# Optimization experiments

Hardware: AMD Instinct MI355X
Metric: run time of the kernel (lower is better)

## Reference

```python
import jax, jax.numpy as jnp
import numpy as np

N_NODES = 50000
N_EDGES = 800000
IN_CH, HIDDEN, OUT_CH = 64, 16, 8


def setup_inputs() -> dict:
    key = jax.random.key(0)
    ks = jax.random.split(key, 8)
    x = jax.random.normal(ks[0], (N_NODES, IN_CH), dtype=jnp.float32)
    edge_index = jax.random.randint(ks[1], (2, N_EDGES), 0, N_NODES, dtype=jnp.int64)
    # SAGEConv params: lin_l (neighbor aggregate, has bias), lin_r (root, no bias)
    s1 = 1.0 / np.sqrt(IN_CH)
    s2 = 1.0 / np.sqrt(HIDDEN)
    W1l = jax.random.uniform(ks[2], (HIDDEN, IN_CH), jnp.float32, -s1, s1)
    W1r = jax.random.uniform(ks[3], (HIDDEN, IN_CH), jnp.float32, -s1, s1)
    b1 = jax.random.uniform(ks[4], (HIDDEN,), jnp.float32, -s1, s1)
    W2l = jax.random.uniform(ks[5], (OUT_CH, HIDDEN), jnp.float32, -s2, s2)
    W2r = jax.random.uniform(ks[6], (OUT_CH, HIDDEN), jnp.float32, -s2, s2)
    b2 = jax.random.uniform(ks[7], (OUT_CH,), jnp.float32, -s2, s2)
    return {"x": x, "W1l": W1l, "W1r": W1r, "b1": b1,
            "W2l": W2l, "W2r": W2r, "b2": b2, "edge_index": edge_index}


def _sage_conv(x, src, dst, Wl, Wr, b, n_nodes):
    # mean-aggregate neighbor features: gather from src, scatter-mean to dst
    msg_sum = jax.ops.segment_sum(x[src], dst, num_segments=n_nodes)  # [N, d]
    deg = jax.ops.segment_sum(jnp.ones((src.shape[0], 1), x.dtype), dst,
                              num_segments=n_nodes)                    # [N, 1]
    aggr = msg_sum / jnp.maximum(deg, 1.0)
    # out = lin_l(aggr) + lin_r(x); bias lives in lin_l
    return aggr @ Wl.T + x @ Wr.T + b


def reference(x, W1l, W1r, b1, W2l, W2r, b2, edge_index):
    src, dst = edge_index[0], edge_index[1]
    n = x.shape[0]
    h = jax.nn.relu(_sage_conv(x, src, dst, W1l, W1r, b1, n))
    # F.dropout(p=0.1, training=self.training): identity in eval mode
    return _sage_conv(h, src, dst, W2l, W2r, b2, n)
```

## Files before the change

kernel.cpp:

```cpp
#include <hip/hip_runtime.h>

#define IN_CH 64
#define HID   16
#define OUTC  8
#define BINSHIFT 6
#define BINCAP  (1 << BINSHIFT)
#define CHUNK   2048

typedef _Float16 half2_t __attribute__((ext_vector_type(2)));
typedef _Float16 half8_t __attribute__((ext_vector_type(8)));


__global__ __launch_bounds__(256) void build_xform(
    const float* __restrict__ x,
    const int*   __restrict__ esrc,
    const int*   __restrict__ edst,
    const float* __restrict__ W1l,
    const float* __restrict__ W1r,
    const float* __restrict__ b1,
    int* __restrict__ cur,
    unsigned short* __restrict__ adj,
    _Float16* __restrict__ y1h,
    float* __restrict__ r1,
    int n_nodes, int n_edges, int nb_scatter)
{
    __shared__ __align__(16) float sWl[HID * 68];
    __shared__ __align__(16) float sWr[HID * 68];
    __shared__ __align__(16) float sx[16 * 68];
    __shared__ float sb1[HID];

    int b   = blockIdx.x;
    int tid = threadIdx.x;

    if (b < nb_scatter) {
        int slice = b & 7;
        int chunk = b >> 3;
        int lo = (int)(((long long)slice       * n_nodes) >> 3);
        int hi = (int)(((long long)(slice + 1) * n_nodes) >> 3);
        int base = chunk * CHUNK;
#pragma unroll
        for (int j = 0; j < CHUNK / 256; ++j) {
            int e = base + j * 256 + tid;
            if (e < n_edges) {
                int d = edst[e];
                if (d >= lo && d < hi) {
                    int pos = atomicAdd(&cur[d], 1);
                    if (pos < BINCAP)
                        adj[((size_t)d << BINSHIFT) + pos] =
                            (unsigned short)esrc[e];
                }
            }
        }
        return;
    }

    for (int i = tid; i < HID * IN_CH; i += 256) {
        int c = i >> 6, k = i & 63;
        sWl[c * 68 + k] = W1l[i];
        sWr[c * 68 + k] = W1r[i];
    }
    if (tid < HID) sb1[tid] = b1[tid];

    int nl   = tid >> 4;
    int c    = tid & 15;
    int node = (b - nb_scatter) * 16 + nl;

    if (node < n_nodes)
        *(float4*)&sx[nl * 68 + c * 4] =
            *(const float4*)&x[(size_t)node * IN_CH + c * 4];
    __syncthreads();
    if (node >= n_nodes) return;

    float accL = 0.f, accR = 0.f;
#pragma unroll
    for (int k4 = 0; k4 < 16; ++k4) {
        float4 xv = *(const float4*)&sx [nl * 68 + k4 * 4];
        float4 wl = *(const float4*)&sWl[c  * 68 + k4 * 4];
        float4 wr = *(const float4*)&sWr[c  * 68 + k4 * 4];
        accL = fmaf(xv.x, wl.x, accL); accL = fmaf(xv.y, wl.y, accL);
        accL = fmaf(xv.z, wl.z, accL); accL = fmaf(xv.w, wl.w, accL);
        accR = fmaf(xv.x, wr.x, accR); accR = fmaf(xv.y, wr.y, accR);
        accR = fmaf(xv.z, wr.z, accR); accR = fmaf(xv.w, wr.w, accR);
    }
    y1h[(size_t)node * HID + c] = (_Float16)accL;
    r1 [(size_t)node * HID + c] = accR + sb1[c];
}

#define ACC8(v)                                                          \
    do {                                                                 \
        half2_t p01 = {(v).s0, (v).s1}, p23 = {(v).s2, (v).s3};          \
        half2_t p45 = {(v).s4, (v).s5}, p67 = {(v).s6, (v).s7};          \
        s0 = __builtin_amdgcn_fdot2(p01, k10, s0, false);                \
        s1 = __builtin_amdgcn_fdot2(p01, k01, s1, false);                \
        s2 = __builtin_amdgcn_fdot2(p23, k10, s2, false);                \
        s3 = __builtin_amdgcn_fdot2(p23, k01, s3, false);                \
        s4 = __builtin_amdgcn_fdot2(p45, k10, s4, false);                \
        s5 = __builtin_amdgcn_fdot2(p45, k01, s5, false);                \
        s6 = __builtin_amdgcn_fdot2(p67, k10, s6, false);                \
        s7 = __builtin_amdgcn_fdot2(p67, k01, s7, false);                \
    } while (0)

__global__ __launch_bounds__(256) void fused_gather(
    const float* __restrict__ r1,
    const _Float16* __restrict__ y1h,
    const int*   __restrict__ cur,
    const unsigned short* __restrict__ adj,
    const float* __restrict__ W2l, const float* __restrict__ W2r,
    const float* __restrict__ b2,
    _Float16* __restrict__ y2h, float* __restrict__ r2out,
    int n_nodes)
{
    __shared__ float sW2l[HID * OUTC];
    __shared__ float sW2r[HID * OUTC];
    __shared__ float sb2[OUTC];
    __shared__ float sh[32 * 17];

    int tid = threadIdx.x;
    for (int i = tid; i < HID * OUTC; i += 256) {
        int o = i >> 4, k = i & 15;
        sW2l[k * OUTC + o] = W2l[i];
        sW2r[k * OUTC + o] = W2r[i];
    }
    if (tid < OUTC) sb2[tid] = b2[tid];

    int nl   = tid >> 3;
    int t    = tid & 7;
    int h    = t >> 2;
    int ep   = t & 3;
    int node = blockIdx.x * 32 + nl;
    bool real = node < n_nodes;

    const half2_t k10 = {(_Float16)1.f, (_Float16)0.f};
    const half2_t k01 = {(_Float16)0.f, (_Float16)1.f};

    if (real) {
        int deg = cur[node];
        if (deg > BINCAP) deg = BINCAP;
        int iters = deg >> 2;
        float s0 = 0.f, s1 = 0.f, s2 = 0.f, s3 = 0.f;
        float s4 = 0.f, s5 = 0.f, s6 = 0.f, s7 = 0.f;
        const _Float16* yq = y1h + h * 8;
        const unsigned short* row = adj + ((size_t)node << BINSHIFT);
        const ushort4* ap = (const ushort4*)row;
        for (int it = ep; it < iters; it += 4) {
            ushort4 s = ap[it];
            half8_t v0 = *(const half8_t*)(yq + (size_t)s.x * HID);
            half8_t v1 = *(const half8_t*)(yq + (size_t)s.y * HID);
            half8_t v2 = *(const half8_t*)(yq + (size_t)s.z * HID);
            half8_t v3 = *(const half8_t*)(yq + (size_t)s.w * HID);
            ACC8(v0); ACC8(v1); ACC8(v2); ACC8(v3);
        }
        for (int g = (iters << 2) + ep; g < deg; g += 4) {
            half8_t v = *(const half8_t*)(yq + (size_t)row[g] * HID);
            ACC8(v);
        }
        s0 += __shfl_xor(s0, 1); s0 += __shfl_xor(s0, 2);
        s1 += __shfl_xor(s1, 1); s1 += __shfl_xor(s1, 2);
        s2 += __shfl_xor(s2, 1); s2 += __shfl_xor(s2, 2);
        s3 += __shfl_xor(s3, 1); s3 += __shfl_xor(s3, 2);
        s4 += __shfl_xor(s4, 1); s4 += __shfl_xor(s4, 2);
        s5 += __shfl_xor(s5, 1); s5 += __shfl_xor(s5, 2);
        s6 += __shfl_xor(s6, 1); s6 += __shfl_xor(s6, 2);
        s7 += __shfl_xor(s7, 1); s7 += __shfl_xor(s7, 2);

        if (ep == 0) {
            float inv = 1.0f / fmaxf((float)deg, 1.0f);
            const float* rr = &r1[(size_t)node * HID + h * 8];
            float4 ra = *(const float4*)(rr);
            float4 rb = *(const float4*)(rr + 4);
            float* shp = &sh[nl * 17 + h * 8];
            shp[0] = fmaxf(fmaf(s0, inv, ra.x), 0.f);
            shp[1] = fmaxf(fmaf(s1, inv, ra.y), 0.f);
            shp[2] = fmaxf(fmaf(s2, inv, ra.z), 0.f);
            shp[3] = fmaxf(fmaf(s3, inv, ra.w), 0.f);
            shp[4] = fmaxf(fmaf(s4, inv, rb.x), 0.f);
            shp[5] = fmaxf(fmaf(s5, inv, rb.y), 0.f);
            shp[6] = fmaxf(fmaf(s6, inv, rb.z), 0.f);
            shp[7] = fmaxf(fmaf(s7, inv, rb.w), 0.f);
        }
    }
    __syncthreads();
    if (!real) return;

    const float* hrow = &sh[nl * 17];
    float al = 0.f, ar = sb2[t];
#pragma unroll
    for (int k = 0; k < HID; ++k) {
        float hv = hrow[k];
        al = fmaf(hv, sW2l[k * OUTC + t], al);
        ar = fmaf(hv, sW2r[k * OUTC + t], ar);
    }
    y2h[(size_t)node * OUTC + t] = (_Float16)al;
    r2out[(size_t)node * OUTC + t] = ar;
}

__global__ __launch_bounds__(256) void gather_out(
    const _Float16* __restrict__ y2h,
    const int*   __restrict__ cur,
    const unsigned short* __restrict__ adj,
    float* __restrict__ out,
    int n_nodes)
{
    int tid  = threadIdx.x;
    int node = blockIdx.x * 64 + (tid >> 2);
    if (node >= n_nodes) return;
    int ep = tid & 3;

    int deg = cur[node];
    if (deg > BINCAP) deg = BINCAP;
    int iters = deg >> 2;
    const unsigned short* row = adj + ((size_t)node << BINSHIFT);
    const ushort4* ap = (const ushort4*)row;

    const half2_t k10 = {(_Float16)1.f, (_Float16)0.f};
    const half2_t k01 = {(_Float16)0.f, (_Float16)1.f};

    float s0 = 0.f, s1 = 0.f, s2 = 0.f, s3 = 0.f;
    float s4 = 0.f, s5 = 0.f, s6 = 0.f, s7 = 0.f;
    for (int it = ep; it < iters; it += 4) {
        ushort4 s = ap[it];
        half8_t v0 = *(const half8_t*)(y2h + (size_t)s.x * OUTC);
        half8_t v1 = *(const half8_t*)(y2h + (size_t)s.y * OUTC);
        half8_t v2 = *(const half8_t*)(y2h + (size_t)s.z * OUTC);
        half8_t v3 = *(const half8_t*)(y2h + (size_t)s.w * OUTC);
        ACC8(v0); ACC8(v1); ACC8(v2); ACC8(v3);
    }
    for (int g = (iters << 2) + ep; g < deg; g += 4) {
        half8_t v = *(const half8_t*)(y2h + (size_t)row[g] * OUTC);
        ACC8(v);
    }
    s0 += __shfl_xor(s0, 1); s0 += __shfl_xor(s0, 2);
    s1 += __shfl_xor(s1, 1); s1 += __shfl_xor(s1, 2);
    s2 += __shfl_xor(s2, 1); s2 += __shfl_xor(s2, 2);
    s3 += __shfl_xor(s3, 1); s3 += __shfl_xor(s3, 2);
    s4 += __shfl_xor(s4, 1); s4 += __shfl_xor(s4, 2);
    s5 += __shfl_xor(s5, 1); s5 += __shfl_xor(s5, 2);
    s6 += __shfl_xor(s6, 1); s6 += __shfl_xor(s6, 2);
    s7 += __shfl_xor(s7, 1); s7 += __shfl_xor(s7, 2);
    if (ep != 0) return;

    float inv = 1.0f / fmaxf((float)deg, 1.0f);
    float* op = out + (size_t)node * OUTC;
    float4 c0 = *(float4*)op;
    float4 c1 = *(float4*)(op + 4);
    c0.x = fmaf(s0, inv, c0.x); c0.y = fmaf(s1, inv, c0.y);
    c0.z = fmaf(s2, inv, c0.z); c0.w = fmaf(s3, inv, c0.w);
    c1.x = fmaf(s4, inv, c1.x); c1.y = fmaf(s5, inv, c1.y);
    c1.z = fmaf(s6, inv, c1.z); c1.w = fmaf(s7, inv, c1.w);
    *(float4*)op = c0;
    *(float4*)(op + 4) = c1;
}

extern "C" void kernel_launch(void* const* d_in, const int* in_sizes, int n_in,
                              void* d_out, int out_size, void* d_ws, size_t ws_size,
                              hipStream_t stream)
{
    const float* x   = (const float*)d_in[0];
    const float* W1l = (const float*)d_in[1];
    const float* W1r = (const float*)d_in[2];
    const float* b1  = (const float*)d_in[3];
    const float* W2l = (const float*)d_in[4];
    const float* W2r = (const float*)d_in[5];
    const float* b2  = (const float*)d_in[6];
    const int*   ei  = (const int*)d_in[7];

    int n_nodes = in_sizes[0] / IN_CH;
    int n_edges = in_sizes[7] / 2;
    const int* esrc = ei;
    const int* edst = ei + n_edges;

    float* out = (float*)d_out;

    char* wsb = (char*)d_ws;
    _Float16* y1h = (_Float16*)wsb;
    _Float16* y2h = y1h + (size_t)n_nodes * HID;
    float* r1 = (float*)(y2h + (size_t)n_nodes * OUTC);
    int* cur  = (int*)(r1 + (size_t)n_nodes * HID);
    unsigned short* adj = (unsigned short*)(cur + n_nodes);

    dim3 blk(256);
    int n_chunks   = (n_edges + CHUNK - 1) / CHUNK;
    int nb_scatter = n_chunks * 8;
    int nb_node    = (n_nodes + 15) / 16;

    hipMemsetAsync(cur, 0, (size_t)n_nodes * sizeof(int), stream);

    build_xform<<<dim3(nb_scatter + nb_node), blk, 0, stream>>>(
        x, esrc, edst, W1l, W1r, b1, cur, adj, y1h, r1,
        n_nodes, n_edges, nb_scatter);

    fused_gather<<<dim3((n_nodes + 31) / 32), blk, 0, stream>>>(
        r1, y1h, cur, adj, W2l, W2r, b2, y2h, out, n_nodes);

    gather_out<<<dim3((n_nodes + 63) / 64), blk, 0, stream>>>(
        y2h, cur, adj, out, n_nodes);
}
```

Before: 132.2 us.

## Replace per-node global atomics with two-pass slice partitioning for adjacency build

Edge scatter becomes a two-level counting sort. Partition blocks first histogram destinations into 256-node slices in shared memory, then reserve space with one global atomic per slice and write packed (src, local dst) words into per-slice buffers. A new bin_build kernel then builds each slice's fixed-capacity adjacency bins in LDS and writes them out with coalesced stores. This removes the repeated 8x read of the edge list and the per-edge global atomics on cur, at the cost of an extra kernel launch and an intermediate buffer. It also relies on gcnt having exactly 256 entries, one per slice (ns=196 here), and on slices not overflowing BCAP.

```diff
diff --git a/kernel.cpp b/kernel.cpp
--- a/kernel.cpp
+++ b/kernel.cpp
@@ -5,7 +5,11 @@
 #define OUTC  8
 #define BINSHIFT 6
 #define BINCAP  (1 << BINSHIFT)
-#define CHUNK   2048
+
+#define CHUNK_A     4096
+#define SLICE_SHIFT 8
+#define SLICE_NODES 256
+#define BCAP        6144
 
 typedef _Float16 half2_t __attribute__((ext_vector_type(2)));
 typedef _Float16 half8_t __attribute__((ext_vector_type(8)));
@@ -18,37 +22,48 @@
     const float* __restrict__ W1l,
     const float* __restrict__ W1r,
     const float* __restrict__ b1,
-    int* __restrict__ cur,
-    unsigned short* __restrict__ adj,
+    int* __restrict__ gcnt,
+    unsigned int* __restrict__ gbuf,
     _Float16* __restrict__ y1h,
     float* __restrict__ r1,
-    int n_nodes, int n_edges, int nb_scatter)
+    int n_nodes, int n_edges, int nb_part)
 {
     __shared__ __align__(16) float sWl[HID * 68];
     __shared__ __align__(16) float sWr[HID * 68];
     __shared__ __align__(16) float sx[16 * 68];
     __shared__ float sb1[HID];
+    __shared__ int shist[SLICE_NODES];
+    __shared__ int scurs[SLICE_NODES];
 
     int b   = blockIdx.x;
     int tid = threadIdx.x;
 
-    if (b < nb_scatter) {
-        int slice = b & 7;
-        int chunk = b >> 3;
-        int lo = (int)(((long long)slice       * n_nodes) >> 3);
-        int hi = (int)(((long long)(slice + 1) * n_nodes) >> 3);
-        int base = chunk * CHUNK;
+    if (b < nb_part) {
+        int base = b * CHUNK_A;
+        shist[tid] = 0;
+        __syncthreads();
 #pragma unroll
-        for (int j = 0; j < CHUNK / 256; ++j) {
+        for (int j = 0; j < CHUNK_A / 256; ++j) {
+            int e = base + j * 256 + tid;
+            if (e < n_edges)
+                atomicAdd(&shist[edst[e] >> SLICE_SHIFT], 1);
+        }
+        __syncthreads();
+        int h = shist[tid];
+        if (h) scurs[tid] = atomicAdd(&gcnt[tid], h);
+        __syncthreads();
+#pragma unroll
+        for (int j = 0; j < CHUNK_A / 256; ++j) {
             int e = base + j * 256 + tid;
             if (e < n_edges) {
-                int d = edst[e];
-                if (d >= lo && d < hi) {
-                    int pos = atomicAdd(&cur[d], 1);
-                    if (pos < BINCAP)
-                        adj[((size_t)d << BINSHIFT) + pos] =
-                            (unsigned short)esrc[e];
-                }
+                int d  = edst[e];
+                int s  = esrc[e];
+                int bk = d >> SLICE_SHIFT;
+                int pos = atomicAdd(&scurs[bk], 1);
+                if (pos < BCAP)
+                    gbuf[(size_t)bk * BCAP + pos] =
+                        (unsigned)(s & 0xFFFF) |
+                        ((unsigned)(d & (SLICE_NODES - 1)) << 16);
             }
         }
         return;
@@ -63,7 +78,7 @@
 
     int nl   = tid >> 4;
     int c    = tid & 15;
-    int node = (b - nb_scatter) * 16 + nl;
+    int node = (b - nb_part) * 16 + nl;
 
     if (node < n_nodes)
         *(float4*)&sx[nl * 68 + c * 4] =
@@ -84,6 +99,46 @@
     }
     y1h[(size_t)node * HID + c] = (_Float16)accL;
     r1 [(size_t)node * HID + c] = accR + sb1[c];
+}
+
+__global__ __launch_bounds__(256) void bin_build(
+    const int* __restrict__ gcnt,
+    const unsigned int* __restrict__ gbuf,
+    int* __restrict__ cur,
+    unsigned short* __restrict__ adj,
+    int n_nodes)
+{
+    __shared__ int scnt[SLICE_NODES];
+    __shared__ __align__(16) unsigned short bins[SLICE_NODES * BINCAP];
+
+    int b   = blockIdx.x;
+    int tid = threadIdx.x;
+
+    scnt[tid] = 0;
+    __syncthreads();
+
+    int eb = gcnt[b];
+    if (eb > BCAP) eb = BCAP;
+    const unsigned int* bp = gbuf + (size_t)b * BCAP;
+    for (int i = tid; i < eb; i += 256) {
+        unsigned p = bp[i];
+        int dl  = p >> 16;
+        int pos = atomicAdd(&scnt[dl], 1);
+        if (pos < BINCAP)
+            bins[(dl << BINSHIFT) + pos] = (unsigned short)(p & 0xFFFF);
+    }
+    __syncthreads();
+
+    int node0  = b << SLICE_SHIFT;
+    int nvalid = n_nodes - node0;
+    if (nvalid > SLICE_NODES) nvalid = SLICE_NODES;
+
+    if (tid < nvalid) cur[node0 + tid] = scnt[tid];
+
+    int nv = nvalid << 3;
+    for (int i = tid; i < nv; i += 256)
+        *(uint4*)(adj + ((size_t)node0 << BINSHIFT) + ((size_t)i << 3)) =
+            *(const uint4*)&bins[(size_t)i << 3];
 }
 
 #define ACC8(v)                                                          \
@@ -277,17 +332,21 @@
     float* r1 = (float*)(y2h + (size_t)n_nodes * OUTC);
     int* cur  = (int*)(r1 + (size_t)n_nodes * HID);
     unsigned short* adj = (unsigned short*)(cur + n_nodes);
+    int* gcnt = (int*)(adj + ((size_t)n_nodes << BINSHIFT));
+    unsigned int* gbuf = (unsigned int*)(gcnt + SLICE_NODES);
 
     dim3 blk(256);
-    int n_chunks   = (n_edges + CHUNK - 1) / CHUNK;
-    int nb_scatter = n_chunks * 8;
-    int nb_node    = (n_nodes + 15) / 16;
-
-    hipMemsetAsync(cur, 0, (size_t)n_nodes * sizeof(int), stream);
-
-    build_xform<<<dim3(nb_scatter + nb_node), blk, 0, stream>>>(
-        x, esrc, edst, W1l, W1r, b1, cur, adj, y1h, r1,
-        n_nodes, n_edges, nb_scatter);
+    int nb_part = (n_edges + CHUNK_A - 1) / CHUNK_A;
+    int nb_node = (n_nodes + 15) / 16;
+    int ns      = (n_nodes + SLICE_NODES - 1) >> SLICE_SHIFT;
+
+    hipMemsetAsync(gcnt, 0, SLICE_NODES * sizeof(int), stream);
+
+    build_xform<<<dim3(nb_part + nb_node), blk, 0, stream>>>(
+        x, esrc, edst, W1l, W1r, b1, gcnt, gbuf, y1h, r1,
+        n_nodes, n_edges, nb_part);
+
+    bin_build<<<dim3(ns), blk, 0, stream>>>(gcnt, gbuf, cur, adj, n_nodes);
 
     fused_gather<<<dim3((n_nodes + 31) / 32), blk, 0, stream>>>(
         r1, y1h, cur, adj, W2l, W2r, b2, y2h, out, n_nodes);
```

Measured after the change: 119.3 us. 1.11x faster.
